# Performance work log

Hardware: AMD Instinct MI355X
Metric: run time of the kernel (lower is better)

Reference implementation:

```python
import jax, jax.numpy as jnp
import numpy as np

NUM_GROUPS = 8
K = 2


def setup_inputs() -> dict:
    key = jax.random.key(0)
    k1, k2, k3 = jax.random.split(key, 3)
    b, l, d = 4, 4096, 2048
    g, k = NUM_GROUPS, K
    hdg = d // g  # 256
    x = jax.random.normal(k1, (b, l, d), dtype=jnp.float32)
    Wg = jax.random.normal(k2, (d, g), dtype=jnp.float32) * 0.02  # gate (no bias)
    Wm = jax.random.normal(k3, (k * hdg, k * hdg), dtype=jnp.float32) * 0.02  # inner Linear
    bm = jnp.zeros((k * hdg,), dtype=jnp.float32)
    return {"x": x, "Wg": Wg, "Wm": Wm, "bm": bm}


def reference(x, Wg, Wm, bm):
    b, l, d = x.shape
    g, k = NUM_GROUPS, K
    hdg = d // g
    # gate: softmax + topk over groups
    S = jax.nn.softmax(x @ Wg, axis=-1)            # [b, l, g]
    G, I = jax.lax.top_k(S, k)                     # [b, l, k] each
    x4 = x.reshape(b, l, g, hdg)
    # gather selected feature groups
    sel = jnp.take_along_axis(x4, I[..., None], axis=2)  # [b, l, k, hdg]
    h = (G[..., None] * sel).reshape(b, l, k * hdg)
    # inner model (Linear)
    h = h @ Wm + bm
    h = h.reshape(b, l, k, hdg)
    # scatter back into original groups
    bi = jnp.arange(b)[:, None, None]
    li = jnp.arange(l)[None, :, None]
    out = x4.at[bi, li, I].set(h)
    return out.reshape(b, l, d)
```

## Files before the change

### kernel.cpp

```cpp
#include <hip/hip_runtime.h>
#include <hip/hip_bf16.h>

#define NTOK   16384
#define DIM    2048
#define NGRP   8
#define HDG    256
#define NIN    512

typedef float f32x4 __attribute__((ext_vector_type(4)));
typedef short bf16x8 __attribute__((ext_vector_type(8)));

static __device__ __forceinline__ unsigned short f2bf(float f) {
    unsigned int u = __builtin_bit_cast(unsigned int, f);
    u = (u + 0x7fffu + ((u >> 16) & 1u)) >> 16;
    return (unsigned short)u;
}

__global__ __launch_bounds__(256) void prep_wm(const float* __restrict__ Wm,
                                               ushort* __restrict__ WmT) {
    __shared__ float tile[64][65];
    const int bk = blockIdx.x * 64;
    const int bn = blockIdx.y * 64;
    const int t = threadIdx.x;
    const int r = t >> 4;
    const int c = (t & 15) * 4;
#pragma unroll
    for (int i = 0; i < 4; i++) {
        const float4 v = *(const float4*)&Wm[(bk + r + i * 16) * 512 + bn + c];
        tile[r + i * 16][c + 0] = v.x;
        tile[r + i * 16][c + 1] = v.y;
        tile[r + i * 16][c + 2] = v.z;
        tile[r + i * 16][c + 3] = v.w;
    }
    __syncthreads();
#pragma unroll
    for (int i = 0; i < 4; i++) {
        const int n = r + i * 16;
        ushort4 o;
        o.x = f2bf(tile[c + 0][n]);
        o.y = f2bf(tile[c + 1][n]);
        o.z = f2bf(tile[c + 2][n]);
        o.w = f2bf(tile[c + 3][n]);
        *(ushort4*)&WmT[(bn + n) * 512 + bk + c] = o;
    }
}

__global__ __launch_bounds__(256, 3) void gate_gather(
        const float* __restrict__ x, const float* __restrict__ Wg,
        float* __restrict__ out, ushort* __restrict__ hbuf,
        int* __restrict__ Isel) {
    const int t = threadIdx.x;
    const int lane = t & 63;
    const int wave = t >> 6;
    const int tok0 = blockIdx.x * 8;

    __shared__ float red[8][4][8];
    __shared__ float gateF[8][2];
    __shared__ int   gateI[8][2];

    int4 xa[16];
#pragma unroll
    for (int tt = 0; tt < 8; tt++) {
        xa[2 * tt]     = *(const int4*)&x[(tok0 + tt) * DIM + t * 8];
        xa[2 * tt + 1] = *(const int4*)&x[(tok0 + tt) * DIM + t * 8 + 4];
    }
    float wgr[8][8];
#pragma unroll
    for (int j = 0; j < 8; j++) {
        const float4 a = *(const float4*)&Wg[(t * 8 + j) * 8];
        const float4 b = *(const float4*)&Wg[(t * 8 + j) * 8 + 4];
        wgr[j][0] = a.x; wgr[j][1] = a.y; wgr[j][2] = a.z; wgr[j][3] = a.w;
        wgr[j][4] = b.x; wgr[j][5] = b.y; wgr[j][6] = b.z; wgr[j][7] = b.w;
    }

    const bool s0 = lane & 1;
    const bool s1 = lane & 2;
    const bool s2 = lane & 4;

#pragma unroll
    for (int tt = 0; tt < 8; tt++) {
        const float* xr = (const float*)&xa[2 * tt];
        float acc[8];
#pragma unroll
        for (int g = 0; g < 8; g++) acc[g] = 0.f;
#pragma unroll
        for (int j = 0; j < 8; j++)
#pragma unroll
            for (int g = 0; g < 8; g++)
                acc[g] = fmaf(xr[j], wgr[j][g], acc[g]);
        float n_[4];
#pragma unroll
        for (int j = 0; j < 4; j++) {
            const float keep = s0 ? acc[2 * j + 1] : acc[2 * j];
            const float send = s0 ? acc[2 * j] : acc[2 * j + 1];
            n_[j] = keep + __shfl_xor(send, 1, 64);
        }
        float m_[2];
#pragma unroll
        for (int j = 0; j < 2; j++) {
            const float keep = s1 ? n_[2 * j + 1] : n_[2 * j];
            const float send = s1 ? n_[2 * j] : n_[2 * j + 1];
            m_[j] = keep + __shfl_xor(send, 2, 64);
        }
        float v;
        {
            const float keep = s2 ? m_[1] : m_[0];
            const float send = s2 ? m_[0] : m_[1];
            v = keep + __shfl_xor(send, 4, 64);
        }
        v += __shfl_xor(v, 8, 64);
        v += __shfl_xor(v, 16, 64);
        v += __shfl_xor(v, 32, 64);
        if (lane < 8) red[tt][wave][lane] = v;
    }
    __syncthreads();

    {
        const int ll = lane & 31;
        const int tok_local = wave * 2 + (lane >> 5);

        float v = red[tok_local][ll >> 3][ll & 7];
        v += __shfl_xor(v, 8, 64);
        v += __shfl_xor(v, 16, 64);
        float c[8];
        c[0] = v;
        c[1] = __shfl_xor(c[0], 1, 64);
        c[2] = __shfl_xor(c[0], 2, 64);
        c[3] = __shfl_xor(c[1], 2, 64);
        c[4] = __shfl_xor(c[0], 4, 64);
        c[5] = __shfl_xor(c[1], 4, 64);
        c[6] = __shfl_xor(c[2], 4, 64);
        c[7] = __shfl_xor(c[3], 4, 64);
        const int gbase = ll & 7;

        float m = c[0];
#pragma unroll
        for (int j = 1; j < 8; j++) m = fmaxf(m, c[j]);
        float sum = 0.f;
#pragma unroll
        for (int j = 0; j < 8; j++) sum += __expf(c[j] - m);
        int i0 = 8; float v0 = -3.4e38f;
#pragma unroll
        for (int j = 0; j < 8; j++) {
            const int g = gbase ^ j;
            if (c[j] > v0 || (c[j] == v0 && g < i0)) { v0 = c[j]; i0 = g; }
        }
        int i1 = 8; float v1 = -3.4e38f;
#pragma unroll
        for (int j = 0; j < 8; j++) {
            const int g = gbase ^ j;
            if (g != i0 && (c[j] > v1 || (c[j] == v1 && g < i1))) { v1 = c[j]; i1 = g; }
        }
        const float inv = 1.0f / sum;
        if (ll == 0) {
            gateF[tok_local][0] = __expf(v0 - m) * inv;
            gateF[tok_local][1] = __expf(v1 - m) * inv;
            gateI[tok_local][0] = i0;
            gateI[tok_local][1] = i1;
            int2 sp; sp.x = i0; sp.y = i1;
            *(int2*)&Isel[(tok0 + tok_local) * 2] = sp;
        }
    }
    __syncthreads();

    const int jg = t >> 5;
    const int off = (t & 31) * 8;
#pragma unroll
    for (int tt = 0; tt < 8; tt++) {
        const int tok = tok0 + tt;
        const int i0 = gateI[tt][0];
        const int i1 = gateI[tt][1];
        const float* xr = (const float*)&xa[2 * tt];
        if (jg == i0 || jg == i1) {
            const float gv  = (jg == i0) ? gateF[tt][0] : gateF[tt][1];
            const int slot  = (jg == i0) ? 0 : 1;
            int4 pk;
            pk.x = (int)f2bf(gv * xr[0]) | ((int)f2bf(gv * xr[1]) << 16);
            pk.y = (int)f2bf(gv * xr[2]) | ((int)f2bf(gv * xr[3]) << 16);
            pk.z = (int)f2bf(gv * xr[4]) | ((int)f2bf(gv * xr[5]) << 16);
            pk.w = (int)f2bf(gv * xr[6]) | ((int)f2bf(gv * xr[7]) << 16);
            *(int4*)&hbuf[tok * NIN + slot * HDG + off] = pk;
        } else {
            *(float4*)&out[tok * DIM + t * 8]     = *(const float4*)&xr[0];
            *(float4*)&out[tok * DIM + t * 8 + 4] = *(const float4*)&xr[4];
        }
    }
}

__global__ __launch_bounds__(256) void gemm_scatter(
        const ushort* __restrict__ h, const ushort* __restrict__ WmT,
        const float* __restrict__ bm, const int* __restrict__ Isel,
        float* __restrict__ out) {
    __shared__ ushort Hs[2][128][40];
    __shared__ ushort Ws[2][128][40];
    const int t = threadIdx.x;
    const int lane = t & 63;
    const int wave = t >> 6;
    const int wn = (wave >> 1) * 64;
    const int wt = (wave & 1) * 64;
    const int n_blk = blockIdx.x * 128;
    const int tok_blk = blockIdx.y * 128;

    const int sr = t >> 2;
    const int sc = (t & 3) * 8;

    const ushort* hp0 = &h[(tok_blk + sr) * 512 + sc];
    const ushort* hp1 = hp0 + 64 * 512;
    const ushort* wp0 = &WmT[(n_blk + sr) * 512 + sc];
    const ushort* wp1 = wp0 + 64 * 512;

    int4 rh0[3], rh1[3], rw0[3], rw1[3];
#pragma unroll
    for (int p = 0; p < 2; p++) {
        const int off = p * 32;
        rh0[p] = *(const int4*)(hp0 + off);
        rh1[p] = *(const int4*)(hp1 + off);
        rw0[p] = *(const int4*)(wp0 + off);
        rw1[p] = *(const int4*)(wp1 + off);
    }

    f32x4 acc[4][4];
#pragma unroll
    for (int i = 0; i < 4; i++)
#pragma unroll
        for (int j = 0; j < 4; j++)
            acc[i][j] = (f32x4){0.f, 0.f, 0.f, 0.f};

    const int fr = lane & 15;
    const int kh = (lane >> 4) * 8;

#pragma unroll
    for (int k = 0; k < 16; ++k) {
        const int b = k & 1;
        const int s = k % 3;
        *(int4*)&Hs[b][sr][sc]      = rh0[s];
        *(int4*)&Hs[b][sr + 64][sc] = rh1[s];
        *(int4*)&Ws[b][sr][sc]      = rw0[s];
        *(int4*)&Ws[b][sr + 64][sc] = rw1[s];
        __syncthreads();
        if (k + 2 < 16) {
            const int s2 = (k + 2) % 3;
            const int off = (k + 2) * 32;
            rh0[s2] = *(const int4*)(hp0 + off);
            rh1[s2] = *(const int4*)(hp1 + off);
            rw0[s2] = *(const int4*)(wp0 + off);
            rw1[s2] = *(const int4*)(wp1 + off);
        }
        bf16x8 av[4], bv[4];
#pragma unroll
        for (int i = 0; i < 4; i++) av[i] = *(const bf16x8*)&Ws[b][wn + i * 16 + fr][kh];
#pragma unroll
        for (int j = 0; j < 4; j++) bv[j] = *(const bf16x8*)&Hs[b][wt + j * 16 + fr][kh];
#pragma unroll
        for (int i = 0; i < 4; i++)
#pragma unroll
            for (int j = 0; j < 4; j++)
                acc[i][j] = __builtin_amdgcn_mfma_f32_16x16x32_bf16(
                    av[i], bv[j], acc[i][j], 0, 0, 0);
    }

    const int rq = (lane >> 4) * 4;
    const int n_base = n_blk + wn;
    const int s = n_base >> 8;
    const int n_off_base = (n_base & 255) + rq;
    float4 bmv[4];
#pragma unroll
    for (int i = 0; i < 4; i++) bmv[i] = *(const float4*)&bm[n_base + i * 16 + rq];
#pragma unroll
    for (int j = 0; j < 4; j++) {
        const int tok = tok_blk + wt + j * 16 + fr;
        const int2 sel = *(const int2*)&Isel[tok * 2];
        const int grp = s ? sel.y : sel.x;
        float* op = &out[tok * DIM + grp * HDG + n_off_base];
#pragma unroll
        for (int i = 0; i < 4; i++) {
            float4 o;
            o.x = acc[i][j][0] + bmv[i].x;
            o.y = acc[i][j][1] + bmv[i].y;
            o.z = acc[i][j][2] + bmv[i].z;
            o.w = acc[i][j][3] + bmv[i].w;
            *(float4*)&op[i * 16] = o;
        }
    }
}

extern "C" void kernel_launch(void* const* d_in, const int* in_sizes, int n_in,
                              void* d_out, int out_size, void* d_ws, size_t ws_size,
                              hipStream_t stream) {
    const float* x  = (const float*)d_in[0];
    const float* Wg = (const float*)d_in[1];
    const float* Wm = (const float*)d_in[2];
    const float* bm = (const float*)d_in[3];
    float* out = (float*)d_out;

    char* ws = (char*)d_ws;
    ushort* hbuf = (ushort*)ws;
    ushort* WmT  = (ushort*)(ws + (size_t)16 * 1024 * 1024);
    int*    Isel = (int*)(ws + (size_t)16 * 1024 * 1024 + 512 * 1024);

    prep_wm<<<dim3(8, 8), 256, 0, stream>>>(Wm, WmT);
    gate_gather<<<NTOK / 8, 256, 0, stream>>>(x, Wg, out, hbuf, Isel);
    gemm_scatter<<<dim3(NIN / 128, NTOK / 128), 256, 0, stream>>>(hbuf, WmT, bm, Isel, out);
}
```

Measured before the change: 303.7 us.

## Split gate/gather into a gating kernel and a separate scatter-copy kernel

After: 320.6 us. 1.06x slower.

```diff
diff --git a/kernel.cpp b/kernel.cpp
--- a/kernel.cpp
+++ b/kernel.cpp
@@ -45,25 +45,16 @@
     }
 }
 
-__global__ __launch_bounds__(256, 3) void gate_gather(
+__global__ __launch_bounds__(256) void gate_kernel(
         const float* __restrict__ x, const float* __restrict__ Wg,
-        float* __restrict__ out, ushort* __restrict__ hbuf,
-        int* __restrict__ Isel) {
+        int* __restrict__ Isel, float* __restrict__ gvals) {
     const int t = threadIdx.x;
     const int lane = t & 63;
     const int wave = t >> 6;
     const int tok0 = blockIdx.x * 8;
 
     __shared__ float red[8][4][8];
-    __shared__ float gateF[8][2];
-    __shared__ int   gateI[8][2];
-
-    int4 xa[16];
-#pragma unroll
-    for (int tt = 0; tt < 8; tt++) {
-        xa[2 * tt]     = *(const int4*)&x[(tok0 + tt) * DIM + t * 8];
-        xa[2 * tt + 1] = *(const int4*)&x[(tok0 + tt) * DIM + t * 8 + 4];
-    }
+
     float wgr[8][8];
 #pragma unroll
     for (int j = 0; j < 8; j++) {
@@ -73,13 +64,21 @@
         wgr[j][4] = b.x; wgr[j][5] = b.y; wgr[j][6] = b.z; wgr[j][7] = b.w;
     }
 
+    int4 xa[3][2];
+#pragma unroll
+    for (int p = 0; p < 2; p++) {
+        xa[p][0] = *(const int4*)&x[(tok0 + p) * DIM + t * 8];
+        xa[p][1] = *(const int4*)&x[(tok0 + p) * DIM + t * 8 + 4];
+    }
+
     const bool s0 = lane & 1;
     const bool s1 = lane & 2;
     const bool s2 = lane & 4;
 
 #pragma unroll
     for (int tt = 0; tt < 8; tt++) {
-        const float* xr = (const float*)&xa[2 * tt];
+        const int slot = tt % 3;
+        const float* xr = (const float*)&xa[slot][0];
         float acc[8];
 #pragma unroll
         for (int g = 0; g < 8; g++) acc[g] = 0.f;
@@ -88,6 +87,11 @@
 #pragma unroll
             for (int g = 0; g < 8; g++)
                 acc[g] = fmaf(xr[j], wgr[j][g], acc[g]);
+        if (tt + 2 < 8) {
+            const int ps = (tt + 2) % 3;
+            xa[ps][0] = *(const int4*)&x[(tok0 + tt + 2) * DIM + t * 8];
+            xa[ps][1] = *(const int4*)&x[(tok0 + tt + 2) * DIM + t * 8 + 4];
+        }
         float n_[4];
 #pragma unroll
         for (int j = 0; j < 4; j++) {
@@ -115,74 +119,75 @@
     }
     __syncthreads();
 
-    {
-        const int ll = lane & 31;
-        const int tok_local = wave * 2 + (lane >> 5);
-
-        float v = red[tok_local][ll >> 3][ll & 7];
-        v += __shfl_xor(v, 8, 64);
-        v += __shfl_xor(v, 16, 64);
-        float c[8];
-        c[0] = v;
-        c[1] = __shfl_xor(c[0], 1, 64);
-        c[2] = __shfl_xor(c[0], 2, 64);
-        c[3] = __shfl_xor(c[1], 2, 64);
-        c[4] = __shfl_xor(c[0], 4, 64);
-        c[5] = __shfl_xor(c[1], 4, 64);
-        c[6] = __shfl_xor(c[2], 4, 64);
-        c[7] = __shfl_xor(c[3], 4, 64);
-        const int gbase = ll & 7;
-
-        float m = c[0];
-#pragma unroll
-        for (int j = 1; j < 8; j++) m = fmaxf(m, c[j]);
-        float sum = 0.f;
-#pragma unroll
-        for (int j = 0; j < 8; j++) sum += __expf(c[j] - m);
-        int i0 = 8; float v0 = -3.4e38f;
-#pragma unroll
-        for (int j = 0; j < 8; j++) {
-            const int g = gbase ^ j;
-            if (c[j] > v0 || (c[j] == v0 && g < i0)) { v0 = c[j]; i0 = g; }
-        }
-        int i1 = 8; float v1 = -3.4e38f;
-#pragma unroll
-        for (int j = 0; j < 8; j++) {
-            const int g = gbase ^ j;
-            if (g != i0 && (c[j] > v1 || (c[j] == v1 && g < i1))) { v1 = c[j]; i1 = g; }
-        }
-        const float inv = 1.0f / sum;
-        if (ll == 0) {
-            gateF[tok_local][0] = __expf(v0 - m) * inv;
-            gateF[tok_local][1] = __expf(v1 - m) * inv;
-            gateI[tok_local][0] = i0;
-            gateI[tok_local][1] = i1;
-            int2 sp; sp.x = i0; sp.y = i1;
-            *(int2*)&Isel[(tok0 + tok_local) * 2] = sp;
-        }
-    }
-    __syncthreads();
-
-    const int jg = t >> 5;
-    const int off = (t & 31) * 8;
-#pragma unroll
-    for (int tt = 0; tt < 8; tt++) {
-        const int tok = tok0 + tt;
-        const int i0 = gateI[tt][0];
-        const int i1 = gateI[tt][1];
-        const float* xr = (const float*)&xa[2 * tt];
-        if (jg == i0 || jg == i1) {
-            const float gv  = (jg == i0) ? gateF[tt][0] : gateF[tt][1];
-            const int slot  = (jg == i0) ? 0 : 1;
-            int4 pk;
-            pk.x = (int)f2bf(gv * xr[0]) | ((int)f2bf(gv * xr[1]) << 16);
-            pk.y = (int)f2bf(gv * xr[2]) | ((int)f2bf(gv * xr[3]) << 16);
-            pk.z = (int)f2bf(gv * xr[4]) | ((int)f2bf(gv * xr[5]) << 16);
-            pk.w = (int)f2bf(gv * xr[6]) | ((int)f2bf(gv * xr[7]) << 16);
-            *(int4*)&hbuf[tok * NIN + slot * HDG + off] = pk;
+    const int ll = lane & 31;
+    const int tok_local = wave * 2 + (lane >> 5);
+
+    float v = red[tok_local][ll >> 3][ll & 7];
+    v += __shfl_xor(v, 8, 64);
+    v += __shfl_xor(v, 16, 64);
+    float c[8];
+    c[0] = v;
+    c[1] = __shfl_xor(c[0], 1, 64);
+    c[2] = __shfl_xor(c[0], 2, 64);
+    c[3] = __shfl_xor(c[1], 2, 64);
+    c[4] = __shfl_xor(c[0], 4, 64);
+    c[5] = __shfl_xor(c[1], 4, 64);
+    c[6] = __shfl_xor(c[2], 4, 64);
+    c[7] = __shfl_xor(c[3], 4, 64);
+    const int gbase = ll & 7;
+
+    float m = c[0];
+#pragma unroll
+    for (int j = 1; j < 8; j++) m = fmaxf(m, c[j]);
+    float sum = 0.f;
+#pragma unroll
+    for (int j = 0; j < 8; j++) sum += __expf(c[j] - m);
+    int i0 = 8; float v0 = -3.4e38f;
+#pragma unroll
+    for (int j = 0; j < 8; j++) {
+        const int g = gbase ^ j;
+        if (c[j] > v0 || (c[j] == v0 && g < i0)) { v0 = c[j]; i0 = g; }
+    }
+    int i1 = 8; float v1 = -3.4e38f;
+#pragma unroll
+    for (int j = 0; j < 8; j++) {
+        const int g = gbase ^ j;
+        if (g != i0 && (c[j] > v1 || (c[j] == v1 && g < i1))) { v1 = c[j]; i1 = g; }
+    }
+    const float inv = 1.0f / sum;
+    if (ll == 0) {
+        const int tok = tok0 + tok_local;
+        int2 sp; sp.x = i0; sp.y = i1;
+        *(int2*)&Isel[tok * 2] = sp;
+        float2 gp; gp.x = __expf(v0 - m) * inv; gp.y = __expf(v1 - m) * inv;
+        *(float2*)&gvals[tok * 2] = gp;
+    }
+}
+
+__global__ __launch_bounds__(256) void scatter_copy(
+        const float* __restrict__ x, const int* __restrict__ Isel,
+        const float* __restrict__ gvals, float* __restrict__ out,
+        ushort* __restrict__ hbuf) {
+    const int wave = threadIdx.x >> 6;
+    const int lane = threadIdx.x & 63;
+    const int tok = blockIdx.x * 4 + wave;
+    const int2 sel = *(const int2*)&Isel[tok * 2];
+    const float2 gv = *(const float2*)&gvals[tok * 2];
+    float4 v[8];
+#pragma unroll
+    for (int j = 0; j < 8; j++)
+        v[j] = *(const float4*)&x[tok * DIM + j * HDG + lane * 4];
+#pragma unroll
+    for (int j = 0; j < 8; j++) {
+        if (j == sel.x || j == sel.y) {
+            const float g = (j == sel.x) ? gv.x : gv.y;
+            const int slot = (j == sel.x) ? 0 : 1;
+            int2 pk;
+            pk.x = (int)f2bf(g * v[j].x) | ((int)f2bf(g * v[j].y) << 16);
+            pk.y = (int)f2bf(g * v[j].z) | ((int)f2bf(g * v[j].w) << 16);
+            *(int2*)&hbuf[tok * NIN + slot * HDG + lane * 4] = pk;
         } else {
-            *(float4*)&out[tok * DIM + t * 8]     = *(const float4*)&xr[0];
-            *(float4*)&out[tok * DIM + t * 8 + 4] = *(const float4*)&xr[4];
+            *(float4*)&out[tok * DIM + j * HDG + lane * 4] = v[j];
         }
     }
 }
@@ -294,11 +299,13 @@
     float* out = (float*)d_out;
 
     char* ws = (char*)d_ws;
-    ushort* hbuf = (ushort*)ws;
-    ushort* WmT  = (ushort*)(ws + (size_t)16 * 1024 * 1024);
-    int*    Isel = (int*)(ws + (size_t)16 * 1024 * 1024 + 512 * 1024);
+    ushort* hbuf  = (ushort*)ws;
+    ushort* WmT   = (ushort*)(ws + (size_t)16 * 1024 * 1024);
+    int*    Isel  = (int*)  (ws + (size_t)16 * 1024 * 1024 + 512 * 1024);
+    float*  gvals = (float*)(ws + (size_t)16 * 1024 * 1024 + 640 * 1024);
 
     prep_wm<<<dim3(8, 8), 256, 0, stream>>>(Wm, WmT);
-    gate_gather<<<NTOK / 8, 256, 0, stream>>>(x, Wg, out, hbuf, Isel);
+    gate_kernel<<<NTOK / 8, 256, 0, stream>>>(x, Wg, Isel, gvals);
+    scatter_copy<<<NTOK / 4, 256, 0, stream>>>(x, Isel, gvals, out, hbuf);
     gemm_scatter<<<dim3(NIN / 128, NTOK / 128), 256, 0, stream>>>(hbuf, WmT, bm, Isel, out);
 }
```
